# Kernel optimization log

Hardware: AMD Instinct MI355X
Metric: run time of the kernel (lower is better)

## Reference

```python
import jax, jax.numpy as jnp
import numpy as np

N_EMBD = 1024
N_HEAD = 16
HEAD_DIM = N_EMBD // N_HEAD


def setup_inputs() -> dict:
    key = jax.random.key(0)
    kx, kq, kk, kv, ko = jax.random.split(key, 5)
    s = 1.0 / np.sqrt(N_EMBD)
    return {
        "x": jax.random.normal(kx, (4, 2048, N_EMBD), dtype=jnp.float32),
        "Wq": jax.random.normal(kq, (N_EMBD, N_EMBD), dtype=jnp.float32) * s,
        "Wk": jax.random.normal(kk, (N_EMBD, N_EMBD), dtype=jnp.float32) * s,
        "Wv": jax.random.normal(kv, (N_EMBD, N_EMBD), dtype=jnp.float32) * s,
        "Wo": jax.random.normal(ko, (N_EMBD, N_EMBD), dtype=jnp.float32) * s,
    }


def reference(x, Wq, Wk, Wv, Wo):
    B, T, C = x.shape
    H, D = N_HEAD, HEAD_DIM
    # projections; torch Linear computes x @ W.T
    q = (x @ Wq.T).reshape(B, T, H, D).transpose(0, 2, 1, 3)  # [B,H,T,D]
    k = (x @ Wk.T).reshape(B, T, H, D).transpose(0, 2, 1, 3)
    v = (x @ Wv.T).reshape(B, T, H, D).transpose(0, 2, 1, 3)
    scores = jnp.einsum("bhtd,bhsd->bhts", q, k) / np.sqrt(D).astype(np.float32)
    causal = jnp.tril(jnp.ones((T, T), dtype=bool))
    scores = jnp.where(causal, scores, -jnp.inf)
    attn = jax.nn.softmax(scores, axis=-1)
    out = jnp.einsum("bhts,bhsd->bhtd", attn, v)  # [B,H,T,D]
    out = out.transpose(0, 2, 1, 3).reshape(B, T, C)
    return out @ Wo.T
```

## Files before the change

kernel.cpp:

```cpp
#include <hip/hip_runtime.h>
#include <hip/hip_bf16.h>


typedef __bf16 bf16_t;
typedef __bf16 bf16x4 __attribute__((ext_vector_type(4)));
typedef __bf16 bf16x8 __attribute__((ext_vector_type(8)));
typedef float  f32x4  __attribute__((ext_vector_type(4)));

#define MFMA16(a, b, c) __builtin_amdgcn_mfma_f32_16x16x32_bf16(a, b, c, 0, 0, 0)

__device__ __forceinline__ float exp2_(float x) {
#if __has_builtin(__builtin_amdgcn_exp2f)
    return __builtin_amdgcn_exp2f(x);
#else
    return __expf(x * 0.6931471805599453f);
#endif
}

__device__ __forceinline__ void gload_lds16(const bf16_t* g, bf16_t* l) {
    __builtin_amdgcn_global_load_lds(
        (const __attribute__((address_space(1))) void*)g,
        (__attribute__((address_space(3))) void*)l, 16, 0, 0);
}

__global__ __launch_bounds__(256)
void cast_f32_bf16(const float* __restrict__ in, bf16_t* __restrict__ out, int n8) {
    int i = blockIdx.x * 256 + threadIdx.x;
    if (i >= n8) return;
    const float4* p = (const float4*)in;
    float4 a = p[i * 2], b = p[i * 2 + 1];
    bf16x8 o;
    o[0] = (bf16_t)a.x; o[1] = (bf16_t)a.y; o[2] = (bf16_t)a.z; o[3] = (bf16_t)a.w;
    o[4] = (bf16_t)b.x; o[5] = (bf16_t)b.y; o[6] = (bf16_t)b.z; o[7] = (bf16_t)b.w;
    *(bf16x8*)(out + (size_t)i * 8) = o;
}

__global__ __launch_bounds__(256)
void cast4_f32_bf16(const float* __restrict__ i0, const float* __restrict__ i1,
                    const float* __restrict__ i2, const float* __restrict__ i3,
                    bf16_t* o0, bf16_t* o1, bf16_t* o2, bf16_t* o3, int n8) {
    const float* in = blockIdx.y == 0 ? i0 : blockIdx.y == 1 ? i1 : blockIdx.y == 2 ? i2 : i3;
    bf16_t*     out = blockIdx.y == 0 ? o0 : blockIdx.y == 1 ? o1 : blockIdx.y == 2 ? o2 : o3;
    int i = blockIdx.x * 256 + threadIdx.x;
    if (i >= n8) return;
    const float4* p = (const float4*)in;
    float4 a = p[i * 2], b = p[i * 2 + 1];
    bf16x8 o;
    o[0] = (bf16_t)a.x; o[1] = (bf16_t)a.y; o[2] = (bf16_t)a.z; o[3] = (bf16_t)a.w;
    o[4] = (bf16_t)b.x; o[5] = (bf16_t)b.y; o[6] = (bf16_t)b.z; o[7] = (bf16_t)b.w;
    *(bf16x8*)(out + (size_t)i * 8) = o;
}

template<int OUT_BF16>
__global__ __launch_bounds__(256)
void gemm_bt(const bf16_t* __restrict__ A, const bf16_t* __restrict__ B,
             void* __restrict__ Cv, int M, int N, int K) {
    __shared__ bf16_t As[128 * 32];
    __shared__ bf16_t Bs[128 * 32];
    const int tid = threadIdx.x;
    const int lane = tid & 63;
    const int w = tid >> 6;
    const int wm = w >> 1, wn = w & 1;
    const int g = lane >> 4, c = lane & 15;
    const long bm = (long)blockIdx.x * 128;
    const long bn = (long)blockIdx.y * 128;

    f32x4 acc[4][4] = {};

    const int srow = tid >> 2;
    const int scol = (tid & 3) << 3;
    const bf16_t* Ag = A + (bm + srow) * (long)K + scol;
    const bf16_t* Bg = B + (bn + srow) * (long)K + scol;
    bf16_t* AsW = As + tid * 8;
    bf16_t* BsW = Bs + tid * 8;

    for (int k0 = 0; k0 < K; k0 += 32) {
        gload_lds16(Ag + k0,                 AsW);
        gload_lds16(Ag + k0 + (long)64 * K,  AsW + 2048);
        gload_lds16(Bg + k0,                 BsW);
        gload_lds16(Bg + k0 + (long)64 * K,  BsW + 2048);
        __syncthreads();
        bf16x8 af[4], bfr[4];
        #pragma unroll
        for (int m = 0; m < 4; ++m)
            af[m] = *(const bf16x8*)(As + (wm * 64 + m * 16 + c) * 32 + g * 8);
        #pragma unroll
        for (int n = 0; n < 4; ++n)
            bfr[n] = *(const bf16x8*)(Bs + (wn * 64 + n * 16 + c) * 32 + g * 8);
        #pragma unroll
        for (int m = 0; m < 4; ++m)
            #pragma unroll
            for (int n = 0; n < 4; ++n)
                acc[m][n] = MFMA16(af[m], bfr[n], acc[m][n]);
        __syncthreads();
    }
    #pragma unroll
    for (int m = 0; m < 4; ++m)
        #pragma unroll
        for (int n = 0; n < 4; ++n)
            #pragma unroll
            for (int i = 0; i < 4; ++i) {
                long row = bm + wm * 64 + m * 16 + g * 4 + i;
                long col = bn + wn * 64 + n * 16 + c;
                float v = acc[m][n][i];
                if (OUT_BF16) ((bf16_t*)Cv)[row * N + col] = (bf16_t)v;
                else          ((float*)Cv)[row * N + col]  = v;
            }
}


__device__ __forceinline__ void stage_K(const bf16_t* Kp, long rowb, int kb, int hcol,
                                        bf16_t* Kbuf, int tid) {
    int row = tid >> 3;
    int lb  = (tid & 7) ^ (row & 7);
    gload_lds16(Kp + (rowb + kb + row) * 3072 + hcol + lb * 8, Kbuf + tid * 8);
}

__device__ __forceinline__ bf16x8 load_V8(const bf16_t* Vp, long rowb, int kb,
                                          int hcol, int tid) {
    const int d  = tid & 63;
    const int k0 = (tid >> 6) * 8;
    bf16x8 v;
    #pragma unroll
    for (int j = 0; j < 8; ++j)
        v[j] = Vp[(rowb + kb + k0 + j) * 3072 + hcol + d];
    return v;
}

__device__ __forceinline__ void write_V8(bf16_t* Vbuf, int tid, bf16x8 v) {
    const int d  = tid & 63;
    const int k0 = (tid >> 6) * 8;
    *(bf16x8*)&Vbuf[d * 72 + k0] = v;
}

__global__ __launch_bounds__(512, 4)
void attn_kernel(const bf16_t* __restrict__ Qp, const bf16_t* __restrict__ Kp,
                 const bf16_t* __restrict__ Vp, bf16_t* __restrict__ O) {
    __shared__ bf16_t Ks[2][64 * 64];
    __shared__ bf16_t Vts[2][64 * 72];
    __shared__ bf16_t PW[8][16 * 72];

    const int tid = threadIdx.x, lane = tid & 63, w = tid >> 6;
    const int g = lane >> 4, c = lane & 15;
    const int bh = blockIdx.x, bx = blockIdx.y;
    const int b = bh >> 4, h = bh & 15;
    const long rowb = (long)b * 2048;
    const int hcol = h * 64;
    const float QSCL = 0.18033688011112042f;

    for (int pass = 0; pass < 2; ++pass) {
        const int q0  = pass ? (15 - bx) : bx;
        const int qlo = q0 * 128 + w * 16;
        const int nkt = 2 * q0 + 2;

        bf16x8 qf[2];
        #pragma unroll
        for (int ks = 0; ks < 2; ++ks) {
            qf[ks] = *(const bf16x8*)(Qp + (rowb + qlo + c) * 3072 +
                                      hcol + ks * 32 + g * 8);
            #pragma unroll
            for (int j = 0; j < 8; ++j)
                qf[ks][j] = (bf16_t)((float)qf[ks][j] * QSCL);
        }

        float m_r = -1e30f, l_r = 0.f;
        f32x4 acc[4] = {};

        stage_K(Kp, rowb, 0, hcol, Ks[0], tid);
        write_V8(Vts[0], tid, load_V8(Vp, rowb, 0, hcol, tid));
        __syncthreads();

        for (int t = 0; t < nkt; ++t) {
            const int cur = t & 1;
            const int kb = t * 64;
            const bool pre = (t + 1 < nkt);
            bf16x8 vreg;
            if (pre) {
                stage_K(Kp, rowb, kb + 64, hcol, Ks[cur ^ 1], tid);
                vreg = load_V8(Vp, rowb, kb + 64, hcol, tid);
            }

            if (kb <= qlo + 15) {
                f32x4 sacc[4] = {};
                __builtin_amdgcn_s_setprio(1);
                #pragma unroll
                for (int nt = 0; nt < 4; ++nt) {
                    const int row = nt * 16 + c;
                    #pragma unroll
                    for (int ks = 0; ks < 2; ++ks) {
                        bf16x8 kf = *(const bf16x8*)&Ks[cur][row * 64 +
                                        (((ks * 4 + g) ^ (c & 7)) * 8)];
                        sacc[nt] = MFMA16(kf, qf[ks], sacc[nt]);
                    }
                }
                __builtin_amdgcn_s_setprio(0);
                if (kb + 63 > qlo) {
                    const int q = qlo + c;
                    #pragma unroll
                    for (int nt = 0; nt < 4; ++nt)
                        #pragma unroll
                        for (int i = 0; i < 4; ++i) {
                            int key = kb + nt * 16 + g * 4 + i;
                            if (key > q) sacc[nt][i] = -1e30f;
                        }
                }

                float mx01a = fmaxf(sacc[0][0], sacc[0][1]);
                float mx01b = fmaxf(sacc[0][2], sacc[0][3]);
                float mx11a = fmaxf(sacc[1][0], sacc[1][1]);
                float mx11b = fmaxf(sacc[1][2], sacc[1][3]);
                float mx21a = fmaxf(sacc[2][0], sacc[2][1]);
                float mx21b = fmaxf(sacc[2][2], sacc[2][3]);
                float mx31a = fmaxf(sacc[3][0], sacc[3][1]);
                float mx31b = fmaxf(sacc[3][2], sacc[3][3]);
                float mx = fmaxf(fmaxf(fmaxf(mx01a, mx01b), fmaxf(mx11a, mx11b)),
                                 fmaxf(fmaxf(mx21a, mx21b), fmaxf(mx31a, mx31b)));
                mx = fmaxf(mx, __shfl_xor(mx, 16, 64));
                mx = fmaxf(mx, __shfl_xor(mx, 32, 64));
                if (__any(mx > m_r + 8.f)) {
                    float mnew = fmaxf(m_r, mx);
                    float scl = exp2_(m_r - mnew);
                    #pragma unroll
                    for (int nt = 0; nt < 4; ++nt)
                        acc[nt] *= scl;
                    l_r *= scl;
                    m_r = mnew;
                }
                float rsn[4];
                #pragma unroll
                for (int nt = 0; nt < 4; ++nt) {
                    #pragma unroll
                    for (int i = 0; i < 4; ++i)
                        sacc[nt][i] = exp2_(sacc[nt][i] - m_r);
                    rsn[nt] = (sacc[nt][0] + sacc[nt][1]) + (sacc[nt][2] + sacc[nt][3]);
                }
                float rs = (rsn[0] + rsn[1]) + (rsn[2] + rsn[3]);
                rs += __shfl_xor(rs, 16, 64);
                rs += __shfl_xor(rs, 32, 64);
                l_r += rs;

                #pragma unroll
                for (int nt = 0; nt < 4; ++nt) {
                    bf16x4 t4;
                    #pragma unroll
                    for (int i = 0; i < 4; ++i) t4[i] = (bf16_t)sacc[nt][i];
                    *(bf16x4*)&PW[w][c * 72 + nt * 16 + g * 4] = t4;
                }

                __builtin_amdgcn_s_setprio(1);
                #pragma unroll
                for (int ks = 0; ks < 2; ++ks) {
                    bf16x8 pf = *(const bf16x8*)&PW[w][c * 72 + ks * 32 + g * 8];
                    #pragma unroll
                    for (int nt = 0; nt < 4; ++nt) {
                        bf16x8 vf = *(const bf16x8*)&Vts[cur][(nt * 16 + c) * 72 +
                                                              ks * 32 + g * 8];
                        acc[nt] = MFMA16(vf, pf, acc[nt]);
                    }
                }
                __builtin_amdgcn_s_setprio(0);
            }

            if (pre) write_V8(Vts[cur ^ 1], tid, vreg);
            __syncthreads();
        }

        {
            float rl = __builtin_amdgcn_rcpf(l_r);
            #pragma unroll
            for (int nt = 0; nt < 4; ++nt) {
                bf16x4 t4;
                #pragma unroll
                for (int i = 0; i < 4; ++i) t4[i] = (bf16_t)(acc[nt][i] * rl);
                *(bf16x4*)&PW[w][c * 72 + nt * 16 + g * 4] = t4;
            }
        }
        #pragma unroll
        for (int p = 0; p < 2; ++p) {
            int row = p * 8 + (lane >> 3);
            int ch  = (lane & 7) * 8;
            bf16x8 v = *(const bf16x8*)&PW[w][row * 72 + ch];
            *(bf16x8*)&O[(rowb + qlo + row) * 1024 + hcol + ch] = v;
        }
    }
}

extern "C" void kernel_launch(void* const* d_in, const int* in_sizes, int n_in,
                              void* d_out, int out_size, void* d_ws, size_t ws_size,
                              hipStream_t stream) {
    const float* x  = (const float*)d_in[0];
    const float* Wq = (const float*)d_in[1];
    const float* Wk = (const float*)d_in[2];
    const float* Wv = (const float*)d_in[3];
    const float* Wo = (const float*)d_in[4];

    const int M = 8192;
    const int C = 1024;

    char* ws = (char*)d_ws;
    bf16_t* xb   = (bf16_t*)(ws);
    bf16_t* wqkv = (bf16_t*)(ws + ((size_t)16 << 20));
    bf16_t* wob  = (bf16_t*)(ws + ((size_t)22 << 20));
    bf16_t* qkv  = (bf16_t*)(ws + ((size_t)24 << 20));
    bf16_t* aob  = (bf16_t*)(ws + ((size_t)72 << 20));

    cast_f32_bf16<<<(M * C / 8) / 256, 256, 0, stream>>>(x, xb, M * C / 8);
    cast4_f32_bf16<<<dim3((C * C / 8) / 256, 4), 256, 0, stream>>>(
        Wq, Wk, Wv, Wo,
        wqkv, wqkv + (size_t)(C * C), wqkv + (size_t)(2 * C * C), wob, C * C / 8);

    gemm_bt<1><<<dim3(M / 128, 3072 / 128), 256, 0, stream>>>(xb, wqkv, qkv, M, 3072, C);

    attn_kernel<<<dim3(64, 8), 512, 0, stream>>>(
        qkv, qkv + 1024, qkv + 2048, aob);

    gemm_bt<0><<<dim3(M / 128, C / 128), 256, 0, stream>>>(aob, wob, d_out, M, C, C);
}
```

Baseline: 186.8 us.

## Process 32 query rows per wave to double K/V tile reuse

Each wave now computes two 16-row query fragments against every staged K/V tile, so each block covers a 256-row query tile in one pass instead of two balanced 128-row passes. Sharing each K and V fragment load across two MFMAs is meant to cut LDS and global traffic per unit of attention work. In exchange, the paired-tile load balancing is replaced by a largest-first ordering, per-block work becomes more uneven, and register pressure roughly doubles under the 512x4 launch bound, which may cause spills.

```diff
diff --git a/kernel.cpp b/kernel.cpp
--- a/kernel.cpp
+++ b/kernel.cpp
@@ -138,150 +138,170 @@
                  const bf16_t* __restrict__ Vp, bf16_t* __restrict__ O) {
     __shared__ bf16_t Ks[2][64 * 64];
     __shared__ bf16_t Vts[2][64 * 72];
-    __shared__ bf16_t PW[8][16 * 72];
+    __shared__ bf16_t PW[8][32 * 72];
 
     const int tid = threadIdx.x, lane = tid & 63, w = tid >> 6;
     const int g = lane >> 4, c = lane & 15;
-    const int bh = blockIdx.x, bx = blockIdx.y;
+    const int bh = blockIdx.x;
     const int b = bh >> 4, h = bh & 15;
     const long rowb = (long)b * 2048;
     const int hcol = h * 64;
     const float QSCL = 0.18033688011112042f;
 
-    for (int pass = 0; pass < 2; ++pass) {
-        const int q0  = pass ? (15 - bx) : bx;
-        const int qlo = q0 * 128 + w * 16;
-        const int nkt = 2 * q0 + 2;
-
-        bf16x8 qf[2];
+    const int by = blockIdx.y;
+    const int q0 = by < 4 ? 7 - by : by - 4;
+    const int qlo = q0 * 256 + w * 32;
+    const int nkt = 4 * q0 + 4;
+
+    bf16x8 qf[2][2];
+    #pragma unroll
+    for (int m = 0; m < 2; ++m)
         #pragma unroll
         for (int ks = 0; ks < 2; ++ks) {
-            qf[ks] = *(const bf16x8*)(Qp + (rowb + qlo + c) * 3072 +
-                                      hcol + ks * 32 + g * 8);
+            qf[m][ks] = *(const bf16x8*)(Qp + (rowb + qlo + m * 16 + c) * 3072 +
+                                         hcol + ks * 32 + g * 8);
             #pragma unroll
             for (int j = 0; j < 8; ++j)
-                qf[ks][j] = (bf16_t)((float)qf[ks][j] * QSCL);
+                qf[m][ks][j] = (bf16_t)((float)qf[m][ks][j] * QSCL);
         }
 
-        float m_r = -1e30f, l_r = 0.f;
-        f32x4 acc[4] = {};
-
-        stage_K(Kp, rowb, 0, hcol, Ks[0], tid);
-        write_V8(Vts[0], tid, load_V8(Vp, rowb, 0, hcol, tid));
-        __syncthreads();
-
-        for (int t = 0; t < nkt; ++t) {
-            const int cur = t & 1;
-            const int kb = t * 64;
-            const bool pre = (t + 1 < nkt);
-            bf16x8 vreg;
-            if (pre) {
-                stage_K(Kp, rowb, kb + 64, hcol, Ks[cur ^ 1], tid);
-                vreg = load_V8(Vp, rowb, kb + 64, hcol, tid);
-            }
-
-            if (kb <= qlo + 15) {
-                f32x4 sacc[4] = {};
-                __builtin_amdgcn_s_setprio(1);
-                #pragma unroll
-                for (int nt = 0; nt < 4; ++nt) {
-                    const int row = nt * 16 + c;
-                    #pragma unroll
-                    for (int ks = 0; ks < 2; ++ks) {
-                        bf16x8 kf = *(const bf16x8*)&Ks[cur][row * 64 +
-                                        (((ks * 4 + g) ^ (c & 7)) * 8)];
-                        sacc[nt] = MFMA16(kf, qf[ks], sacc[nt]);
-                    }
-                }
-                __builtin_amdgcn_s_setprio(0);
-                if (kb + 63 > qlo) {
-                    const int q = qlo + c;
+    float m_r[2] = {-1e30f, -1e30f};
+    float l_r[2] = {0.f, 0.f};
+    f32x4 acc[2][4] = {};
+
+    stage_K(Kp, rowb, 0, hcol, Ks[0], tid);
+    write_V8(Vts[0], tid, load_V8(Vp, rowb, 0, hcol, tid));
+    __syncthreads();
+
+    for (int t = 0; t < nkt; ++t) {
+        const int cur = t & 1;
+        const int kb = t * 64;
+        const bool pre = (t + 1 < nkt);
+        bf16x8 vreg;
+        if (pre) {
+            stage_K(Kp, rowb, kb + 64, hcol, Ks[cur ^ 1], tid);
+            vreg = load_V8(Vp, rowb, kb + 64, hcol, tid);
+        }
+
+        if (kb <= qlo + 31) {
+            f32x4 sacc[2][4] = {};
+            __builtin_amdgcn_s_setprio(1);
+            #pragma unroll
+            for (int nt = 0; nt < 4; ++nt) {
+                const int row = nt * 16 + c;
+                #pragma unroll
+                for (int ks = 0; ks < 2; ++ks) {
+                    bf16x8 kf = *(const bf16x8*)&Ks[cur][row * 64 +
+                                    (((ks * 4 + g) ^ (c & 7)) * 8)];
+                    sacc[0][nt] = MFMA16(kf, qf[0][ks], sacc[0][nt]);
+                    sacc[1][nt] = MFMA16(kf, qf[1][ks], sacc[1][nt]);
+                }
+            }
+            __builtin_amdgcn_s_setprio(0);
+            if (kb + 63 > qlo) {
+                #pragma unroll
+                for (int m = 0; m < 2; ++m) {
+                    const int q = qlo + m * 16 + c;
                     #pragma unroll
                     for (int nt = 0; nt < 4; ++nt)
                         #pragma unroll
                         for (int i = 0; i < 4; ++i) {
                             int key = kb + nt * 16 + g * 4 + i;
-                            if (key > q) sacc[nt][i] = -1e30f;
+                            if (key > q) sacc[m][nt][i] = -1e30f;
                         }
                 }
-
-                float mx01a = fmaxf(sacc[0][0], sacc[0][1]);
-                float mx01b = fmaxf(sacc[0][2], sacc[0][3]);
-                float mx11a = fmaxf(sacc[1][0], sacc[1][1]);
-                float mx11b = fmaxf(sacc[1][2], sacc[1][3]);
-                float mx21a = fmaxf(sacc[2][0], sacc[2][1]);
-                float mx21b = fmaxf(sacc[2][2], sacc[2][3]);
-                float mx31a = fmaxf(sacc[3][0], sacc[3][1]);
-                float mx31b = fmaxf(sacc[3][2], sacc[3][3]);
-                float mx = fmaxf(fmaxf(fmaxf(mx01a, mx01b), fmaxf(mx11a, mx11b)),
-                                 fmaxf(fmaxf(mx21a, mx21b), fmaxf(mx31a, mx31b)));
-                mx = fmaxf(mx, __shfl_xor(mx, 16, 64));
-                mx = fmaxf(mx, __shfl_xor(mx, 32, 64));
-                if (__any(mx > m_r + 8.f)) {
-                    float mnew = fmaxf(m_r, mx);
-                    float scl = exp2_(m_r - mnew);
+            }
+
+            float mx[2];
+            #pragma unroll
+            for (int m = 0; m < 2; ++m) {
+                float a0 = fmaxf(fmaxf(sacc[m][0][0], sacc[m][0][1]),
+                                 fmaxf(sacc[m][0][2], sacc[m][0][3]));
+                float a1 = fmaxf(fmaxf(sacc[m][1][0], sacc[m][1][1]),
+                                 fmaxf(sacc[m][1][2], sacc[m][1][3]));
+                float a2 = fmaxf(fmaxf(sacc[m][2][0], sacc[m][2][1]),
+                                 fmaxf(sacc[m][2][2], sacc[m][2][3]));
+                float a3 = fmaxf(fmaxf(sacc[m][3][0], sacc[m][3][1]),
+                                 fmaxf(sacc[m][3][2], sacc[m][3][3]));
+                float mm = fmaxf(fmaxf(a0, a1), fmaxf(a2, a3));
+                mm = fmaxf(mm, __shfl_xor(mm, 16, 64));
+                mm = fmaxf(mm, __shfl_xor(mm, 32, 64));
+                mx[m] = mm;
+            }
+            if (__any(fmaxf(mx[0] - m_r[0], mx[1] - m_r[1]) > 8.f)) {
+                #pragma unroll
+                for (int m = 0; m < 2; ++m) {
+                    float mnew = fmaxf(m_r[m], mx[m]);
+                    float scl = exp2_(m_r[m] - mnew);
                     #pragma unroll
                     for (int nt = 0; nt < 4; ++nt)
-                        acc[nt] *= scl;
-                    l_r *= scl;
-                    m_r = mnew;
-                }
+                        acc[m][nt] *= scl;
+                    l_r[m] *= scl;
+                    m_r[m] = mnew;
+                }
+            }
+            #pragma unroll
+            for (int m = 0; m < 2; ++m) {
                 float rsn[4];
                 #pragma unroll
                 for (int nt = 0; nt < 4; ++nt) {
                     #pragma unroll
                     for (int i = 0; i < 4; ++i)
-                        sacc[nt][i] = exp2_(sacc[nt][i] - m_r);
-                    rsn[nt] = (sacc[nt][0] + sacc[nt][1]) + (sacc[nt][2] + sacc[nt][3]);
+                        sacc[m][nt][i] = exp2_(sacc[m][nt][i] - m_r[m]);
+                    rsn[nt] = (sacc[m][nt][0] + sacc[m][nt][1]) +
+                              (sacc[m][nt][2] + sacc[m][nt][3]);
                 }
                 float rs = (rsn[0] + rsn[1]) + (rsn[2] + rsn[3]);
                 rs += __shfl_xor(rs, 16, 64);
                 rs += __shfl_xor(rs, 32, 64);
-                l_r += rs;
+                l_r[m] += rs;
 
                 #pragma unroll
                 for (int nt = 0; nt < 4; ++nt) {
                     bf16x4 t4;
                     #pragma unroll
-                    for (int i = 0; i < 4; ++i) t4[i] = (bf16_t)sacc[nt][i];
-                    *(bf16x4*)&PW[w][c * 72 + nt * 16 + g * 4] = t4;
-                }
-
-                __builtin_amdgcn_s_setprio(1);
-                #pragma unroll
-                for (int ks = 0; ks < 2; ++ks) {
-                    bf16x8 pf = *(const bf16x8*)&PW[w][c * 72 + ks * 32 + g * 8];
-                    #pragma unroll
-                    for (int nt = 0; nt < 4; ++nt) {
-                        bf16x8 vf = *(const bf16x8*)&Vts[cur][(nt * 16 + c) * 72 +
-                                                              ks * 32 + g * 8];
-                        acc[nt] = MFMA16(vf, pf, acc[nt]);
-                    }
-                }
-                __builtin_amdgcn_s_setprio(0);
-            }
-
-            if (pre) write_V8(Vts[cur ^ 1], tid, vreg);
-            __syncthreads();
+                    for (int i = 0; i < 4; ++i) t4[i] = (bf16_t)sacc[m][nt][i];
+                    *(bf16x4*)&PW[w][(m * 16 + c) * 72 + nt * 16 + g * 4] = t4;
+                }
+            }
+
+            __builtin_amdgcn_s_setprio(1);
+            #pragma unroll
+            for (int ks = 0; ks < 2; ++ks) {
+                bf16x8 pf0 = *(const bf16x8*)&PW[w][(c)      * 72 + ks * 32 + g * 8];
+                bf16x8 pf1 = *(const bf16x8*)&PW[w][(16 + c) * 72 + ks * 32 + g * 8];
+                #pragma unroll
+                for (int nt = 0; nt < 4; ++nt) {
+                    bf16x8 vf = *(const bf16x8*)&Vts[cur][(nt * 16 + c) * 72 +
+                                                          ks * 32 + g * 8];
+                    acc[0][nt] = MFMA16(vf, pf0, acc[0][nt]);
+                    acc[1][nt] = MFMA16(vf, pf1, acc[1][nt]);
+                }
+            }
+            __builtin_amdgcn_s_setprio(0);
         }
 
-        {
-            float rl = __builtin_amdgcn_rcpf(l_r);
-            #pragma unroll
-            for (int nt = 0; nt < 4; ++nt) {
-                bf16x4 t4;
-                #pragma unroll
-                for (int i = 0; i < 4; ++i) t4[i] = (bf16_t)(acc[nt][i] * rl);
-                *(bf16x4*)&PW[w][c * 72 + nt * 16 + g * 4] = t4;
-            }
+        if (pre) write_V8(Vts[cur ^ 1], tid, vreg);
+        __syncthreads();
+    }
+
+    #pragma unroll
+    for (int m = 0; m < 2; ++m) {
+        float rl = __builtin_amdgcn_rcpf(l_r[m]);
+        #pragma unroll
+        for (int nt = 0; nt < 4; ++nt) {
+            bf16x4 t4;
+            #pragma unroll
+            for (int i = 0; i < 4; ++i) t4[i] = (bf16_t)(acc[m][nt][i] * rl);
+            *(bf16x4*)&PW[w][(m * 16 + c) * 72 + nt * 16 + g * 4] = t4;
         }
-        #pragma unroll
-        for (int p = 0; p < 2; ++p) {
-            int row = p * 8 + (lane >> 3);
-            int ch  = (lane & 7) * 8;
-            bf16x8 v = *(const bf16x8*)&PW[w][row * 72 + ch];
-            *(bf16x8*)&O[(rowb + qlo + row) * 1024 + hcol + ch] = v;
-        }
+    }
+    #pragma unroll
+    for (int p = 0; p < 4; ++p) {
+        int row = p * 8 + (lane >> 3);
+        int ch  = (lane & 7) * 8;
+        bf16x8 v = *(const bf16x8*)&PW[w][row * 72 + ch];
+        *(bf16x8*)&O[(rowb + qlo + row) * 1024 + hcol + ch] = v;
     }
 }
 
```

Measured after the change: 193.4 us. +3.5%, slower.
